# Optimization experiments

Measured on AMD Instinct MI355X. Metric: run time of the kernel, lower is better.

## Reference

```python
import jax, jax.numpy as jnp
import numpy as np

HIDDEN = 1024
HEADS = 16
HEAD = HIDDEN // HEADS


def _ternary_weight(key, shape):
    g = jax.random.normal(key, shape, dtype=jnp.float32)
    return jnp.where(jnp.abs(g) < 0.6, 0.0, jnp.sign(g)).astype(jnp.float32)


def setup_inputs() -> dict:
    key = jax.random.key(0)
    ks = jax.random.split(key, 10)
    x = jax.random.normal(ks[0], (2, 2048, HIDDEN), dtype=jnp.float32)
    d = {"x": x}
    names = ["q", "k", "v", "o"]
    for i, n in enumerate(names):
        d[f"w_{n}"] = _ternary_weight(ks[1 + i], (HIDDEN, HIDDEN))
        d[f"s_{n}"] = jnp.float32(0.02)  # per-layer dequant scale
        d[f"b_{n}"] = jax.random.normal(ks[5 + i], (HIDDEN,), dtype=jnp.float32) * 0.02
    return d


def _tlin(x, w, s, b):
    # dequantized ternary linear: x @ (s * w).T + b
    return jnp.einsum("bsh,oh->bso", x, w) * s + b


def reference(x, w_q, s_q, b_q, w_k, s_k, b_k, w_v, s_v, b_v, w_o, s_o, b_o):
    B, S, H = x.shape
    def split_heads(t):
        return t.reshape(B, S, HEADS, HEAD).transpose(0, 2, 1, 3)  # [B, nH, S, hd]
    q = split_heads(_tlin(x, w_q, s_q, b_q))
    k = split_heads(_tlin(x, w_k, s_k, b_k))
    v = split_heads(_tlin(x, w_v, s_v, b_v))
    scores = jnp.einsum("bhqd,bhkd->bhqk", q, k) / jnp.sqrt(jnp.float32(HEAD))
    attn = jax.nn.softmax(scores, axis=-1)
    ctx = jnp.einsum("bhqk,bhkd->bhqd", attn, v)
    ctx = ctx.transpose(0, 2, 1, 3).reshape(B, S, H)
    return _tlin(ctx, w_o, s_o, b_o)
```

## Files before the change

kernel.cpp:

```cpp
#include <hip/hip_runtime.h>
#include <hip/hip_bf16.h>

typedef unsigned short u16;
typedef __bf16 bf16x8 __attribute__((ext_vector_type(8)));
typedef __bf16 bf16x4 __attribute__((ext_vector_type(4)));
typedef float f32x4 __attribute__((ext_vector_type(4)));
typedef unsigned short u16x8 __attribute__((ext_vector_type(8)));

__device__ inline u16 f2bf(float f) {
    union { float f; unsigned u; } v; v.f = f;
    unsigned r = v.u + 0x7fffu + ((v.u >> 16) & 1u);
    return (u16)(r >> 16);
}

__global__ void convert_kernel(const float* __restrict__ x,
                               const float* __restrict__ wq, const float* __restrict__ wk,
                               const float* __restrict__ wv, const float* __restrict__ wo,
                               u16* __restrict__ dst) {
    long g = (long)blockIdx.x * blockDim.x + threadIdx.x;
    const float* src; long base;
    const long GX = 1048576, GW = 262144;
    if (g < GX)            { src = x;  base = 0; }
    else if (g < GX + GW)  { src = wq; base = GX; }
    else if (g < GX + 2*GW){ src = wk; base = GX + GW; }
    else if (g < GX + 3*GW){ src = wv; base = GX + 2*GW; }
    else                   { src = wo; base = GX + 3*GW; }
    long rel = g - base;
    float4 v = reinterpret_cast<const float4*>(src)[rel];
    ushort4 o;
    o.x = f2bf(v.x); o.y = f2bf(v.y); o.z = f2bf(v.z); o.w = f2bf(v.w);
    reinterpret_cast<ushort4*>(dst)[g] = o;
}

__device__ inline void gemm_mainloop(const u16* __restrict__ A, const u16* __restrict__ W,
                                     int t0, int n0, u16* As, u16* Bs, f32x4 acc[4][4]) {
    const int tid = threadIdx.x;
    const int wid = tid >> 6, lane = tid & 63, quad = lane >> 4, ln = lane & 15;
    const int wm = wid >> 1, wn = wid & 1;
#pragma unroll
    for (int im = 0; im < 4; im++)
#pragma unroll
        for (int in = 0; in < 4; in++) acc[im][in] = (f32x4){0.f, 0.f, 0.f, 0.f};

    for (int k0 = 0; k0 < 1024; k0 += 64) {
#pragma unroll
        for (int i = 0; i < 4; i++) {
            int chunk = wid * 4 + i;
            int b = chunk * 1024 + lane * 16;
            int row = b >> 7;
            int cb = (b & 127) ^ ((row & 7) << 4);
            const u16* gA = A + (long)(t0 + row) * 1024 + k0 + (cb >> 1);
            const u16* gB = W + (long)(n0 + row) * 1024 + k0 + (cb >> 1);
            __builtin_amdgcn_global_load_lds((const __attribute__((address_space(1))) void*)gA,
                                             (__attribute__((address_space(3))) void*)(As + chunk * 512),
                                             16, 0, 0);
            __builtin_amdgcn_global_load_lds((const __attribute__((address_space(1))) void*)gB,
                                             (__attribute__((address_space(3))) void*)(Bs + chunk * 512),
                                             16, 0, 0);
        }
        __syncthreads();
#pragma unroll
        for (int ks = 0; ks < 2; ks++) {
            bf16x8 af[4], bfr[4];
#pragma unroll
            for (int im = 0; im < 4; im++) {
                int r = wm * 64 + im * 16 + ln;
                int byt = (r * 128 + ks * 64 + quad * 16) ^ ((r & 7) << 4);
                af[im] = *reinterpret_cast<const bf16x8*>((const char*)As + byt);
            }
#pragma unroll
            for (int in = 0; in < 4; in++) {
                int r = wn * 64 + in * 16 + ln;
                int byt = (r * 128 + ks * 64 + quad * 16) ^ ((r & 7) << 4);
                bfr[in] = *reinterpret_cast<const bf16x8*>((const char*)Bs + byt);
            }
#pragma unroll
            for (int im = 0; im < 4; im++)
#pragma unroll
                for (int in = 0; in < 4; in++)
                    acc[im][in] = __builtin_amdgcn_mfma_f32_16x16x32_bf16(af[im], bfr[in], acc[im][in], 0, 0, 0);
        }
        __syncthreads();
    }
}

__global__ void qkv_gemm(const u16* __restrict__ x_bf,
                         const u16* __restrict__ wq, const u16* __restrict__ wk, const u16* __restrict__ wv,
                         const float* __restrict__ sq, const float* __restrict__ sk, const float* __restrict__ sv,
                         const float* __restrict__ bq, const float* __restrict__ bk, const float* __restrict__ bv,
                         u16* __restrict__ q_ws, u16* __restrict__ k_ws, u16* __restrict__ v_ws) {
    __shared__ __align__(16) u16 As[128 * 64];
    __shared__ __align__(16) u16 Bs[128 * 64];
    const int z = blockIdx.z;
    const u16* W   = (z == 0) ? wq : (z == 1) ? wk : wv;
    const float* sp = (z == 0) ? sq : (z == 1) ? sk : sv;
    const float* bp = (z == 0) ? bq : (z == 1) ? bk : bv;
    u16* dst = (z == 0) ? q_ws : (z == 1) ? k_ws : v_ws;
    const float extra = (z == 0) ? 0.125f * 1.44269504088896f : 1.0f;
    const int t0 = blockIdx.x * 128, n0 = blockIdx.y * 128;

    f32x4 acc[4][4];
    gemm_mainloop(x_bf, W, t0, n0, As, Bs, acc);

    const int tid = threadIdx.x;
    const int wid = tid >> 6, lane = tid & 63, quad = lane >> 4, ln = lane & 15;
    const int wm = wid >> 1, wn = wid & 1;
    const float s = sp[0] * extra;
#pragma unroll
    for (int in = 0; in < 4; in++) {
        int col = n0 + wn * 64 + in * 16 + ln;
        float bias = bp[col] * extra;
        int h = col >> 6, d = col & 63;
#pragma unroll
        for (int im = 0; im < 4; im++) {
            int rbase = t0 + wm * 64 + im * 16 + quad * 4;
#pragma unroll
            for (int j = 0; j < 4; j++) {
                int t = rbase + j;
                int b = t >> 11, ss = t & 2047;
                int bh = b * 16 + h;
                float val = acc[im][in][j] * s + bias;
                long idx = (z < 2) ? ((long)(bh * 2048 + ss) * 64 + d)
                                   : ((long)(bh * 64 + d) * 2048 + ss);
                dst[idx] = f2bf(val);
            }
        }
    }
}

#define LDP 72

__global__ void __launch_bounds__(512)
attn_kernel(const u16* __restrict__ q_ws, const u16* __restrict__ k_ws,
            const u16* __restrict__ v_ws, u16* __restrict__ ctx) {
    __shared__ __align__(16) u16 Kb[2][4096];
    __shared__ __align__(16) u16 Vb[2][4096];
    __shared__ u16 Pt[128 * LDP];

    const int tid = threadIdx.x;
    const int wid = tid >> 6, lane = tid & 63, quad = lane >> 4, ln = lane & 15;
    const int bh = blockIdx.y;
    const int q0 = blockIdx.x * 128;
    const u16* qbase = q_ws + (long)bh * 2048 * 64;
    const u16* kbase = k_ws + (long)bh * 2048 * 64;
    const u16* vbase = v_ws + (long)bh * 64 * 2048;

    const int srow = wid * 8 + (lane >> 3);
    const int sel  = 8 * ((lane & 7) ^ ((lane >> 3) & 7));
    const int xr = (ln & 7) << 4;

    bf16x8 aq[2];
#pragma unroll
    for (int ks = 0; ks < 2; ks++)
        aq[ks] = *reinterpret_cast<const bf16x8*>(
            qbase + (long)(q0 + wid * 16 + ln) * 64 + ks * 32 + quad * 8);

    bf16x8 vones;
#pragma unroll
    for (int i = 0; i < 8; i++) vones[i] = (__bf16)1.0f;

    f32x4 acc_o[4];
    f32x4 acc_l = (f32x4){0.f, 0.f, 0.f, 0.f};
#pragma unroll
    for (int dt = 0; dt < 4; dt++) acc_o[dt] = (f32x4){0.f, 0.f, 0.f, 0.f};

    const u16* kp = kbase + (long)srow * 64 + sel;
    const u16* vp = vbase + (long)srow * 2048 + sel;

    __builtin_amdgcn_global_load_lds((const __attribute__((address_space(1))) void*)kp,
                                     (__attribute__((address_space(3))) void*)(&Kb[0][wid * 512]),
                                     16, 0, 0);
    __builtin_amdgcn_global_load_lds((const __attribute__((address_space(1))) void*)vp,
                                     (__attribute__((address_space(3))) void*)(&Vb[0][wid * 512]),
                                     16, 0, 0);
    kp += 4096; vp += 64;
    __syncthreads();

    int cur = 0;
    for (int kt = 0; kt < 2048; kt += 64) {
        if (kt + 64 < 2048) {
            __builtin_amdgcn_global_load_lds((const __attribute__((address_space(1))) void*)kp,
                                             (__attribute__((address_space(3))) void*)(&Kb[cur ^ 1][wid * 512]),
                                             16, 0, 0);
            __builtin_amdgcn_global_load_lds((const __attribute__((address_space(1))) void*)vp,
                                             (__attribute__((address_space(3))) void*)(&Vb[cur ^ 1][wid * 512]),
                                             16, 0, 0);
            kp += 4096; vp += 64;
        }
        const char* Kc = (const char*)(&Kb[cur][0]);
        const char* Vc = (const char*)(&Vb[cur][0]);

#pragma unroll
        for (int k8 = 0; k8 < 4; k8++) {
            bf16x8 a0 = *reinterpret_cast<const bf16x8*>(
                Kc + (k8 * 16 + ln) * 128 + ((quad * 16) ^ xr));
            bf16x8 a1 = *reinterpret_cast<const bf16x8*>(
                Kc + (k8 * 16 + ln) * 128 + ((64 + quad * 16) ^ xr));
            f32x4 t = (f32x4){0.f, 0.f, 0.f, 0.f};
            __builtin_amdgcn_s_setprio(1);
            t = __builtin_amdgcn_mfma_f32_16x16x32_bf16(a0, aq[0], t, 0, 0, 0);
            t = __builtin_amdgcn_mfma_f32_16x16x32_bf16(a1, aq[1], t, 0, 0, 0);
            __builtin_amdgcn_s_setprio(0);
            __bf16 p0 = (__bf16)__builtin_amdgcn_exp2f(t[0]);
            __bf16 p1 = (__bf16)__builtin_amdgcn_exp2f(t[1]);
            __bf16 p2 = (__bf16)__builtin_amdgcn_exp2f(t[2]);
            __bf16 p3 = (__bf16)__builtin_amdgcn_exp2f(t[3]);
            *reinterpret_cast<bf16x4*>(Pt + (wid * 16 + ln) * LDP + k8 * 16 + quad * 4)
                = (bf16x4){p0, p1, p2, p3};
        }

#pragma unroll
        for (int step = 0; step < 2; step++) {
            bf16x8 ap = *reinterpret_cast<const bf16x8*>(
                Pt + (wid * 16 + ln) * LDP + step * 32 + quad * 8);
            bf16x8 bv0 = *reinterpret_cast<const bf16x8*>(
                Vc + (0 * 16 + ln) * 128 + ((step * 64 + quad * 16) ^ xr));
            bf16x8 bv1 = *reinterpret_cast<const bf16x8*>(
                Vc + (1 * 16 + ln) * 128 + ((step * 64 + quad * 16) ^ xr));
            bf16x8 bv2 = *reinterpret_cast<const bf16x8*>(
                Vc + (2 * 16 + ln) * 128 + ((step * 64 + quad * 16) ^ xr));
            bf16x8 bv3 = *reinterpret_cast<const bf16x8*>(
                Vc + (3 * 16 + ln) * 128 + ((step * 64 + quad * 16) ^ xr));
            __builtin_amdgcn_s_setprio(1);
            acc_o[0] = __builtin_amdgcn_mfma_f32_16x16x32_bf16(ap, bv0, acc_o[0], 0, 0, 0);
            acc_o[1] = __builtin_amdgcn_mfma_f32_16x16x32_bf16(ap, bv1, acc_o[1], 0, 0, 0);
            acc_o[2] = __builtin_amdgcn_mfma_f32_16x16x32_bf16(ap, bv2, acc_o[2], 0, 0, 0);
            acc_o[3] = __builtin_amdgcn_mfma_f32_16x16x32_bf16(ap, bv3, acc_o[3], 0, 0, 0);
            acc_l    = __builtin_amdgcn_mfma_f32_16x16x32_bf16(ap, vones, acc_l, 0, 0, 0);
            __builtin_amdgcn_s_setprio(0);
        }
        __syncthreads();
        cur ^= 1;
    }

    const int b = bh >> 4, h = bh & 15;
#pragma unroll
    for (int j = 0; j < 4; j++) {
        float rinv = 1.0f / acc_l[j];
        int t = b * 2048 + q0 + wid * 16 + quad * 4 + j;
#pragma unroll
        for (int dt = 0; dt < 4; dt++) {
            float val = acc_o[dt][j] * rinv;
            ctx[(long)t * 1024 + h * 64 + dt * 16 + ln] = f2bf(val);
        }
    }
}

__global__ void __launch_bounds__(512)
o_gemm(const u16* __restrict__ ctx, const u16* __restrict__ wo,
       const float* __restrict__ so, const float* __restrict__ bo,
       float* __restrict__ out) {
    __shared__ __align__(16) u16 As[2][128 * 64];
    __shared__ __align__(16) u16 Bs[2][128 * 64];
    const int tid = threadIdx.x;
    const int wid = tid >> 6, lane = tid & 63, quad = lane >> 4, ln = lane & 15;
    const int wm = wid >> 2, wn = wid & 3;
    const int t0 = blockIdx.x * 128, n0 = blockIdx.y * 128;

    const bool stA = (wid < 4);
    const u16* gbase = stA ? ctx : wo;
    const int r0 = stA ? t0 : n0;
    const int cbase = (wid & 3) * 4;

    f32x4 acc[4][2];
#pragma unroll
    for (int im = 0; im < 4; im++)
#pragma unroll
        for (int in = 0; in < 2; in++) acc[im][in] = (f32x4){0.f, 0.f, 0.f, 0.f};

    const int sb   = cbase * 1024 + lane * 16;
    const int srow = sb >> 7;
    const int scb  = (sb & 127) ^ ((srow & 7) << 4);

#define O_STAGE(buf, k0)                                                              \
    {                                                                                 \
        const u16* g = gbase + (long)(r0 + srow) * 1024 + (k0) + (scb >> 1);          \
        u16* d = (stA ? &As[buf][0] : &Bs[buf][0]) + cbase * 512;                     \
        _Pragma("unroll")                                                             \
        for (int i = 0; i < 4; i++) {                                                 \
            __builtin_amdgcn_global_load_lds(                                         \
                (const __attribute__((address_space(1))) void*)(g + (long)i * 8 * 1024), \
                (__attribute__((address_space(3))) void*)(d + i * 512), 16, 0, 0);    \
        }                                                                             \
    }

    O_STAGE(0, 0);
    __syncthreads();

    int cur = 0;
    for (int k0 = 0; k0 < 1024; k0 += 64) {
        if (k0 + 64 < 1024) O_STAGE(cur ^ 1, k0 + 64);
        const char* Ac = (const char*)&As[cur][0];
        const char* Bc = (const char*)&Bs[cur][0];
#pragma unroll
        for (int ks = 0; ks < 2; ks++) {
            bf16x8 af[4], bfr[2];
#pragma unroll
            for (int im = 0; im < 4; im++) {
                int r = wm * 64 + im * 16 + ln;
                int byt = (r * 128 + ks * 64 + quad * 16) ^ ((r & 7) << 4);
                af[im] = *reinterpret_cast<const bf16x8*>(Ac + byt);
            }
#pragma unroll
            for (int in = 0; in < 2; in++) {
                int r = wn * 32 + in * 16 + ln;
                int byt = (r * 128 + ks * 64 + quad * 16) ^ ((r & 7) << 4);
                bfr[in] = *reinterpret_cast<const bf16x8*>(Bc + byt);
            }
#pragma unroll
            for (int im = 0; im < 4; im++)
#pragma unroll
                for (int in = 0; in < 2; in++)
                    acc[im][in] = __builtin_amdgcn_mfma_f32_16x16x32_bf16(af[im], bfr[in], acc[im][in], 0, 0, 0);
        }
        __syncthreads();
        cur ^= 1;
    }
#undef O_STAGE

    const float s = so[0];
#pragma unroll
    for (int in = 0; in < 2; in++) {
        int col = n0 + wn * 32 + in * 16 + ln;
        float bias = bo[col];
#pragma unroll
        for (int im = 0; im < 4; im++) {
            int rbase = t0 + wm * 64 + im * 16 + quad * 4;
#pragma unroll
            for (int j = 0; j < 4; j++)
                out[(long)(rbase + j) * 1024 + col] = acc[im][in][j] * s + bias;
        }
    }
}

extern "C" void kernel_launch(void* const* d_in, const int* in_sizes, int n_in,
                              void* d_out, int out_size, void* d_ws, size_t ws_size,
                              hipStream_t stream) {
    const float* x   = (const float*)d_in[0];
    const float* w_q = (const float*)d_in[1];
    const float* s_q = (const float*)d_in[2];
    const float* b_q = (const float*)d_in[3];
    const float* w_k = (const float*)d_in[4];
    const float* s_k = (const float*)d_in[5];
    const float* b_k = (const float*)d_in[6];
    const float* w_v = (const float*)d_in[7];
    const float* s_v = (const float*)d_in[8];
    const float* b_v = (const float*)d_in[9];
    const float* w_o = (const float*)d_in[10];
    const float* s_o = (const float*)d_in[11];
    const float* b_o = (const float*)d_in[12];

    if (ws_size < (size_t)50331648) return;

    u16* ws     = (u16*)d_ws;
    u16* x_bf   = ws;
    u16* wq_bf  = x_bf  + 4194304;
    u16* wk_bf  = wq_bf + 1048576;
    u16* wv_bf  = wk_bf + 1048576;
    u16* wo_bf  = wv_bf + 1048576;
    u16* q_ws   = wo_bf + 1048576;
    u16* k_ws   = q_ws  + 4194304;
    u16* v_ws   = k_ws  + 4194304;
    u16* ctx_ws = v_ws  + 4194304;

    convert_kernel<<<dim3(8192), dim3(256), 0, stream>>>(x, w_q, w_k, w_v, w_o, ws);
    qkv_gemm<<<dim3(32, 8, 3), dim3(256), 0, stream>>>(x_bf, wq_bf, wk_bf, wv_bf,
                                                       s_q, s_k, s_v, b_q, b_k, b_v,
                                                       q_ws, k_ws, v_ws);
    attn_kernel<<<dim3(16, 32), dim3(512), 0, stream>>>(q_ws, k_ws, v_ws, ctx_ws);
    o_gemm<<<dim3(32, 8), dim3(512), 0, stream>>>(ctx_ws, wo_bf, s_o, b_o, (float*)d_out);
}
```

Before: 192.8 us.

## Double-buffer QKV GEMM LDS tiles and use 8 warps with split loaders

The QKV projection GEMM moves from 4 waves with a single LDS buffer to 8 waves with double-buffered A/B tiles. The next K slice is prefetched into the alternate buffer while MFMAs run on the current one. Half the waves load A and half load B, and each wave now computes a 64x32 sub-tile. This aims to hide global-to-LDS latency and add waves per block, at the cost of twice the LDS per block, which may lower occupancy.

```diff
diff --git a/kernel.cpp b/kernel.cpp
--- a/kernel.cpp
+++ b/kernel.cpp
@@ -32,65 +32,14 @@
     reinterpret_cast<ushort4*>(dst)[g] = o;
 }
 
-__device__ inline void gemm_mainloop(const u16* __restrict__ A, const u16* __restrict__ W,
-                                     int t0, int n0, u16* As, u16* Bs, f32x4 acc[4][4]) {
-    const int tid = threadIdx.x;
-    const int wid = tid >> 6, lane = tid & 63, quad = lane >> 4, ln = lane & 15;
-    const int wm = wid >> 1, wn = wid & 1;
-#pragma unroll
-    for (int im = 0; im < 4; im++)
-#pragma unroll
-        for (int in = 0; in < 4; in++) acc[im][in] = (f32x4){0.f, 0.f, 0.f, 0.f};
-
-    for (int k0 = 0; k0 < 1024; k0 += 64) {
-#pragma unroll
-        for (int i = 0; i < 4; i++) {
-            int chunk = wid * 4 + i;
-            int b = chunk * 1024 + lane * 16;
-            int row = b >> 7;
-            int cb = (b & 127) ^ ((row & 7) << 4);
-            const u16* gA = A + (long)(t0 + row) * 1024 + k0 + (cb >> 1);
-            const u16* gB = W + (long)(n0 + row) * 1024 + k0 + (cb >> 1);
-            __builtin_amdgcn_global_load_lds((const __attribute__((address_space(1))) void*)gA,
-                                             (__attribute__((address_space(3))) void*)(As + chunk * 512),
-                                             16, 0, 0);
-            __builtin_amdgcn_global_load_lds((const __attribute__((address_space(1))) void*)gB,
-                                             (__attribute__((address_space(3))) void*)(Bs + chunk * 512),
-                                             16, 0, 0);
-        }
-        __syncthreads();
-#pragma unroll
-        for (int ks = 0; ks < 2; ks++) {
-            bf16x8 af[4], bfr[4];
-#pragma unroll
-            for (int im = 0; im < 4; im++) {
-                int r = wm * 64 + im * 16 + ln;
-                int byt = (r * 128 + ks * 64 + quad * 16) ^ ((r & 7) << 4);
-                af[im] = *reinterpret_cast<const bf16x8*>((const char*)As + byt);
-            }
-#pragma unroll
-            for (int in = 0; in < 4; in++) {
-                int r = wn * 64 + in * 16 + ln;
-                int byt = (r * 128 + ks * 64 + quad * 16) ^ ((r & 7) << 4);
-                bfr[in] = *reinterpret_cast<const bf16x8*>((const char*)Bs + byt);
-            }
-#pragma unroll
-            for (int im = 0; im < 4; im++)
-#pragma unroll
-                for (int in = 0; in < 4; in++)
-                    acc[im][in] = __builtin_amdgcn_mfma_f32_16x16x32_bf16(af[im], bfr[in], acc[im][in], 0, 0, 0);
-        }
-        __syncthreads();
-    }
-}
-
-__global__ void qkv_gemm(const u16* __restrict__ x_bf,
-                         const u16* __restrict__ wq, const u16* __restrict__ wk, const u16* __restrict__ wv,
-                         const float* __restrict__ sq, const float* __restrict__ sk, const float* __restrict__ sv,
-                         const float* __restrict__ bq, const float* __restrict__ bk, const float* __restrict__ bv,
-                         u16* __restrict__ q_ws, u16* __restrict__ k_ws, u16* __restrict__ v_ws) {
-    __shared__ __align__(16) u16 As[128 * 64];
-    __shared__ __align__(16) u16 Bs[128 * 64];
+__global__ void __launch_bounds__(512)
+qkv_gemm(const u16* __restrict__ x_bf,
+         const u16* __restrict__ wq, const u16* __restrict__ wk, const u16* __restrict__ wv,
+         const float* __restrict__ sq, const float* __restrict__ sk, const float* __restrict__ sv,
+         const float* __restrict__ bq, const float* __restrict__ bk, const float* __restrict__ bv,
+         u16* __restrict__ q_ws, u16* __restrict__ k_ws, u16* __restrict__ v_ws) {
+    __shared__ __align__(16) u16 As[2][128 * 64];
+    __shared__ __align__(16) u16 Bs[2][128 * 64];
     const int z = blockIdx.z;
     const u16* W   = (z == 0) ? wq : (z == 1) ? wk : wv;
     const float* sp = (z == 0) ? sq : (z == 1) ? sk : sv;
@@ -99,16 +48,75 @@
     const float extra = (z == 0) ? 0.125f * 1.44269504088896f : 1.0f;
     const int t0 = blockIdx.x * 128, n0 = blockIdx.y * 128;
 
-    f32x4 acc[4][4];
-    gemm_mainloop(x_bf, W, t0, n0, As, Bs, acc);
-
     const int tid = threadIdx.x;
     const int wid = tid >> 6, lane = tid & 63, quad = lane >> 4, ln = lane & 15;
-    const int wm = wid >> 1, wn = wid & 1;
+    const int wm = wid >> 2, wn = wid & 3;
+
+    const bool stA = (wid < 4);
+    const u16* gbase = stA ? x_bf : W;
+    const int r0 = stA ? t0 : n0;
+    const int cbase = (wid & 3) * 4;
+
+    f32x4 acc[4][2];
+#pragma unroll
+    for (int im = 0; im < 4; im++)
+#pragma unroll
+        for (int in = 0; in < 2; in++) acc[im][in] = (f32x4){0.f, 0.f, 0.f, 0.f};
+
+    const int sb   = cbase * 1024 + lane * 16;
+    const int srow = sb >> 7;
+    const int scb  = (sb & 127) ^ ((srow & 7) << 4);
+
+#define Q_STAGE(buf, k0)                                                              \
+    {                                                                                 \
+        const u16* g = gbase + (long)(r0 + srow) * 1024 + (k0) + (scb >> 1);          \
+        u16* d = (stA ? &As[buf][0] : &Bs[buf][0]) + cbase * 512;                     \
+        _Pragma("unroll")                                                             \
+        for (int i = 0; i < 4; i++) {                                                 \
+            __builtin_amdgcn_global_load_lds(                                         \
+                (const __attribute__((address_space(1))) void*)(g + (long)i * 8 * 1024), \
+                (__attribute__((address_space(3))) void*)(d + i * 512), 16, 0, 0);    \
+        }                                                                             \
+    }
+
+    Q_STAGE(0, 0);
+    __syncthreads();
+
+    int cur = 0;
+    for (int k0 = 0; k0 < 1024; k0 += 64) {
+        if (k0 + 64 < 1024) Q_STAGE(cur ^ 1, k0 + 64);
+        const char* Ac = (const char*)&As[cur][0];
+        const char* Bc = (const char*)&Bs[cur][0];
+#pragma unroll
+        for (int ks = 0; ks < 2; ks++) {
+            bf16x8 af[4], bfr[2];
+#pragma unroll
+            for (int im = 0; im < 4; im++) {
+                int r = wm * 64 + im * 16 + ln;
+                int byt = (r * 128 + ks * 64 + quad * 16) ^ ((r & 7) << 4);
+                af[im] = *reinterpret_cast<const bf16x8*>(Ac + byt);
+            }
+#pragma unroll
+            for (int in = 0; in < 2; in++) {
+                int r = wn * 32 + in * 16 + ln;
+                int byt = (r * 128 + ks * 64 + quad * 16) ^ ((r & 7) << 4);
+                bfr[in] = *reinterpret_cast<const bf16x8*>(Bc + byt);
+            }
+#pragma unroll
+            for (int im = 0; im < 4; im++)
+#pragma unroll
+                for (int in = 0; in < 2; in++)
+                    acc[im][in] = __builtin_amdgcn_mfma_f32_16x16x32_bf16(af[im], bfr[in], acc[im][in], 0, 0, 0);
+        }
+        __syncthreads();
+        cur ^= 1;
+    }
+#undef Q_STAGE
+
     const float s = sp[0] * extra;
 #pragma unroll
-    for (int in = 0; in < 4; in++) {
-        int col = n0 + wn * 64 + in * 16 + ln;
+    for (int in = 0; in < 2; in++) {
+        int col = n0 + wn * 32 + in * 16 + ln;
         float bias = bp[col] * extra;
         int h = col >> 6, d = col & 63;
 #pragma unroll
@@ -364,7 +372,7 @@
     u16* ctx_ws = v_ws  + 4194304;
 
     convert_kernel<<<dim3(8192), dim3(256), 0, stream>>>(x, w_q, w_k, w_v, w_o, ws);
-    qkv_gemm<<<dim3(32, 8, 3), dim3(256), 0, stream>>>(x_bf, wq_bf, wk_bf, wv_bf,
+    qkv_gemm<<<dim3(32, 8, 3), dim3(512), 0, stream>>>(x_bf, wq_bf, wk_bf, wv_bf,
                                                        s_q, s_k, s_v, b_q, b_k, b_v,
                                                        q_ws, k_ws, v_ws);
     attn_kernel<<<dim3(16, 32), dim3(512), 0, stream>>>(q_ws, k_ws, v_ws, ctx_ws);
```

Result: no change. 190.7 us (-1.1%).
